# Kernel optimization log

Measured on AMD Instinct MI355X. Metric: run time of the kernel, lower is better.

The kernel has to match this reference:

```python
import jax, jax.numpy as jnp
import numpy as np
import itertools, functools, operator

NUM_RBF = 32
CUTOFF = 5.0
METRIC = (1, 1, 1)


def _count_bits(x):
    return bin(x).count("1")


def _sign_euclidean(a, b):
    a >>= 1
    s = 0
    while a:
        s += _count_bits(a & b)
        a >>= 1
    return 1 if (s & 1) == 0 else -1


def build_cayley(metric):
    """Dense [2^n, 2^n, 2^n] geometric multiplication (Cayley) table, shortlex blade order."""
    n = len(metric)
    blade_sets = itertools.chain.from_iterable(
        itertools.combinations([1 << i for i in range(n)], r) for r in range(n + 1)
    )
    index_to_bitmap = [functools.reduce(operator.or_, t, 0) for t in blade_sets]
    bitmap_to_index = {b: i for i, b in enumerate(index_to_bitmap)}
    N = 2 ** n
    cayley = np.zeros((N, N, N), dtype=np.float32)
    for i in range(N):
        bi = index_to_bitmap[i]
        for j in range(N):
            bj = index_to_bitmap[j]
            sign = _sign_euclidean(bi, bj)
            bm = bi & bj
            k = 0
            while bm:
                if bm & 1:
                    sign *= metric[k]
                k += 1
                bm >>= 1
            cayley[i, bitmap_to_index[bi ^ bj], j] = sign
    return cayley


CAYLEY = jnp.asarray(build_cayley(METRIC))  # [8,8,8], sparse +/-1 structure


def geometric_product(a, b):
    # torch: einsum('...i,ijk,...k->...j', a, cayley, b)
    return jnp.einsum('...i,ijk,...k->...j', a, CAYLEY, b)


def setup_inputs() -> dict:
    key = jax.random.key(0)
    k0, k1, k2, k3, k4, k5 = jax.random.split(key, 6)
    N, E, C = 50000, 800000, 16
    h = jax.random.normal(k0, (N, C, 8), jnp.float32)
    pos = jax.random.uniform(k1, (N, 3), jnp.float32) * 10.0
    edge_index = jax.random.randint(k2, (2, E), 0, N, jnp.int32)
    W_rbf = jax.random.normal(k3, (NUM_RBF, C), jnp.float32) / np.sqrt(NUM_RBF)
    W_out = jax.random.normal(k4, (C, C), jnp.float32) / np.sqrt(C)
    W_sgp = jax.random.normal(k5, (C, C), jnp.float32) / np.sqrt(C)
    return {"h": h, "pos": pos, "edge_index": edge_index,
            "W_rbf": W_rbf, "W_out": W_out, "W_sgp": W_sgp}


def reference(h, pos, edge_index, W_rbf, W_out, W_sgp):
    N, C, B = h.shape
    src, dst = edge_index[0], edge_index[1]

    # relative geometry
    rel = pos[dst] - pos[src]                                  # [E,3]
    dist = jnp.sqrt(jnp.sum(rel * rel, axis=-1) + 1e-12)       # [E]

    # embed unit relative vector as a grade-1 multivector (blades 1..3)
    rel_mv = jnp.zeros((rel.shape[0], 1, B), h.dtype)
    rel_mv = rel_mv.at[:, 0, 1:4].set(rel / dist[:, None])     # [E,1,8]

    # radial weights: gaussian smearing -> linear -> cosine cutoff envelope
    mus = jnp.linspace(0.0, CUTOFF, NUM_RBF, dtype=h.dtype)
    gamma = (NUM_RBF / CUTOFF) ** 2
    rbf = jnp.exp(-gamma * (dist[:, None] - mus) ** 2)         # [E,32]
    env = 0.5 * (jnp.cos(jnp.pi * dist / CUTOFF) + 1.0) * (dist < CUTOFF)
    w_e = (rbf @ W_rbf) * env[:, None]                          # [E,C]

    # equivariant messages: geometric product against edge multivector
    msg = geometric_product(h[src], rel_mv) * w_e[..., None]   # [E,C,8]
    agg = jax.ops.segment_sum(msg, dst, num_segments=N)        # [N,C,8]

    # MVLinear channel mixing (shared across blades)
    out = jnp.einsum('nci,co->noi', agg, W_out)                # [N,C,8]

    # MACE-style higher-order: steerable geometric product self-interaction
    q = jnp.einsum('nci,co->noi', h, W_sgp)                    # [N,C,8]
    return out + geometric_product(out, q)
```

## Files before the change

kernel.cpp:

```cpp
#include <hip/hip_runtime.h>

#define CUTOFF 5.0f
#define GAMMA 40.96f
#define MU_STEP 0.16129032f
#define INV_MU 6.2f
#define PI_F 3.14159265358979f
#define MAXDEG 24


__global__ __launch_bounds__(256) void k_fill_geom(
    const float* __restrict__ pos, const int* __restrict__ ei,
    int* __restrict__ deg, int* __restrict__ rec,
    float4* __restrict__ edata, int E)
{
    int e = blockIdx.x * 256 + threadIdx.x;
    if (e >= E) return;
    int src = ei[e], dst = ei[E + e];
    float dx = pos[dst*3+0] - pos[src*3+0];
    float dy = pos[dst*3+1] - pos[src*3+1];
    float dz = pos[dst*3+2] - pos[src*3+2];
    float d = sqrtf(dx*dx + dy*dy + dz*dz + 1e-12f);
    if (d < CUTOFF) {
        int slot = atomicAdd(&deg[dst], 1);
        if (slot < MAXDEG) {
            const float s = (0.5f * (__cosf(PI_F * d * (1.0f/CUTOFF)) + 1.0f)) / d;
            rec[dst*MAXDEG + slot] = src;
            edata[(size_t)dst*MAXDEG + slot] = make_float4(dx*s, dy*s, dz*s, d);
        }
    }
}

__global__ __launch_bounds__(256) void k_gather_finalize(
    const float* __restrict__ h,
    const int* __restrict__ rec, const int* __restrict__ deg,
    const float4* __restrict__ edata,
    const float* __restrict__ Wrbf, const float* __restrict__ Wout,
    const float* __restrict__ Wsgp, float* __restrict__ out, int N)
{
    __shared__ float s_wr[512];
    __shared__ float s_Wout[256];
    __shared__ float s_Wsgp[256];
    __shared__ float s_agg[16*132];
    __shared__ float s_h[16*132];

    const int t  = threadIdx.x;
    const int nl = t >> 4;
    const int c  = t & 15;
    const int lane  = t & 63;
    const int gbase = lane & 48;
    const long long nodeBase = (long long)blockIdx.x * 16;
    const long long n = nodeBase + nl;

    s_wr[t]       = Wrbf[t];
    s_wr[t + 256] = Wrbf[t + 256];
    s_Wout[t] = Wout[t];
    s_Wsgp[t] = Wsgp[t];

    for (int idx = t; idx < 512; idx += 256) {
        int nn = idx >> 5;
        int r  = idx & 31;
        long long node = nodeBase + nn;
        float4 vh = make_float4(0,0,0,0);
        if (node < N) vh = *(const float4*)(h + node*128 + (long long)r*4);
        *(float4*)(&s_h[nn*132 + r*4]) = vh;
    }
    __syncthreads();

    float m0=0,m1=0,m2=0,m3=0,m4=0,m5=0,m6=0,m7=0;
    if (n < N) {
        const int start = (int)n * MAXDEG;
        const int dg    = min(deg[n], MAXDEG);
        for (int base = 0; base < dg; base += 2) {
            const int i1ok = (base + 1 < dg) ? 1 : 0;
            const int s0 = rec[start + base];
            const int s1 = rec[start + base + i1ok];
            const float4 g0 = edata[start + base];
            const float4 g1 = edata[start + base + i1ok];

            const float4* hp0 = (const float4*)(h + (((long long)s0*16 + c) << 3));
            const float4* hp1 = (const float4*)(h + (((long long)s1*16 + c) << 3));
            const float4 A0 = hp0[0], B0 = hp0[1];
            const float4 A1 = hp1[0], B1 = hp1[1];

            const int kl0 = min(max(0, __float2int_rn(g0.w * INV_MU) - 3), 25);
            const int kl1 = min(max(0, __float2int_rn(g1.w * INV_MU) - 3), 25);

            const int   sel   = c >> 3;
            const float dsel  = sel ? g1.w : g0.w;
            const int   klsel = sel ? kl1 : kl0;
            const float xx = dsel - MU_STEP * (float)(klsel + (c & 7));
            const float ee = __expf(-GAMMA * xx * xx);

            float w0 = 0.0f, w1 = 0.0f;
            #pragma unroll
            for (int j = 0; j < 7; ++j) {
                const float e0 = __shfl(ee, gbase + j);
                const float e1 = __shfl(ee, gbase + 8 + j);
                w0 += e0 * s_wr[(kl0 + j)*16 + c];
                w1 += e1 * s_wr[(kl1 + j)*16 + c];
            }
            w1 *= (float)i1ok;

            m0 += (A0.y*g0.x + A0.z*g0.y + A0.w*g0.z)*w0 + (A1.y*g1.x + A1.z*g1.y + A1.w*g1.z)*w1;
            m1 += (A0.x*g0.x + B0.x*g0.y + B0.y*g0.z)*w0 + (A1.x*g1.x + B1.x*g1.y + B1.y*g1.z)*w1;
            m2 += (A0.x*g0.y - B0.x*g0.x + B0.z*g0.z)*w0 + (A1.x*g1.y - B1.x*g1.x + B1.z*g1.z)*w1;
            m3 += (A0.x*g0.z - B0.y*g0.x - B0.z*g0.y)*w0 + (A1.x*g1.z - B1.y*g1.x - B1.z*g1.y)*w1;
            m4 += (A0.y*g0.y - A0.z*g0.x + B0.w*g0.z)*w0 + (A1.y*g1.y - A1.z*g1.x + B1.w*g1.z)*w1;
            m5 += (A0.y*g0.z - A0.w*g0.x - B0.w*g0.y)*w0 + (A1.y*g1.z - A1.w*g1.x - B1.w*g1.y)*w1;
            m6 += (A0.z*g0.z - A0.w*g0.y + B0.w*g0.x)*w0 + (A1.z*g1.z - A1.w*g1.y + B1.w*g1.x)*w1;
            m7 += (B0.z*g0.x - B0.y*g0.y + B0.x*g0.z)*w0 + (B1.z*g1.x - B1.y*g1.y + B1.x*g1.z)*w1;
        }
    }

    __syncthreads();
    float* ag = &s_agg[nl*132 + c*8];
    *(float4*)(ag)     = make_float4(m0, m1, m2, m3);
    *(float4*)(ag + 4) = make_float4(m4, m5, m6, m7);
    __syncthreads();

    const int o = c;
    const float* A = &s_agg[nl*132];
    const float* H = &s_h[nl*132];

    float o0=0,o1=0,o2=0,o3=0,o4=0,o5=0,o6=0,o7=0;
    float q0=0,q1=0,q2=0,q3=0,q4=0,q5=0,q6=0,q7=0;
    #pragma unroll
    for (int cc = 0; cc < 16; ++cc) {
        const float wo = s_Wout[cc*16 + o];
        const float ws = s_Wsgp[cc*16 + o];
        const float* a  = A + cc*8;
        const float* hh = H + cc*8;
        o0 += a[0]*wo; o1 += a[1]*wo; o2 += a[2]*wo; o3 += a[3]*wo;
        o4 += a[4]*wo; o5 += a[5]*wo; o6 += a[6]*wo; o7 += a[7]*wo;
        q0 += hh[0]*ws; q1 += hh[1]*ws; q2 += hh[2]*ws; q3 += hh[3]*ws;
        q4 += hh[4]*ws; q5 += hh[5]*ws; q6 += hh[6]*ws; q7 += hh[7]*ws;
    }

    const float r0 = o0 + (o0*q0 + o1*q1 + o2*q2 + o3*q3 - o4*q4 - o5*q5 - o6*q6 - o7*q7);
    const float r1 = o1 + (o0*q1 + o1*q0 - o2*q4 - o3*q5 + o4*q2 + o5*q3 - o6*q7 - o7*q6);
    const float r2 = o2 + (o0*q2 + o1*q4 + o2*q0 - o3*q6 - o4*q1 + o5*q7 + o6*q3 + o7*q5);
    const float r3 = o3 + (o0*q3 + o1*q5 + o2*q6 + o3*q0 - o4*q7 - o5*q1 - o6*q2 - o7*q4);
    const float r4 = o4 + (o0*q4 + o1*q2 - o2*q1 + o3*q7 + o4*q0 - o5*q6 + o6*q5 + o7*q3);
    const float r5 = o5 + (o0*q5 + o1*q3 - o2*q7 - o3*q1 + o4*q6 + o5*q0 - o6*q4 - o7*q2);
    const float r6 = o6 + (o0*q6 + o1*q7 + o2*q3 - o3*q2 - o4*q5 + o5*q4 + o6*q0 + o7*q1);
    const float r7 = o7 + (o0*q7 + o1*q6 - o2*q5 + o3*q4 + o4*q3 - o5*q2 + o6*q1 + o7*q0);

    if (n < N) {
        float* op = out + (n*16 + o)*8;
        *(float4*)(op)     = make_float4(r0, r1, r2, r3);
        *(float4*)(op + 4) = make_float4(r4, r5, r6, r7);
    }
}

extern "C" void kernel_launch(void* const* d_in, const int* in_sizes, int n_in,
                              void* d_out, int out_size, void* d_ws, size_t ws_size,
                              hipStream_t stream) {
    const float* h    = (const float*)d_in[0];
    const float* pos  = (const float*)d_in[1];
    const int*   ei   = (const int*)d_in[2];
    const float* Wrbf = (const float*)d_in[3];
    const float* Wout = (const float*)d_in[4];
    const float* Wsgp = (const float*)d_in[5];
    float* out = (float*)d_out;

    const int N = in_sizes[0] / 128;
    const int E = in_sizes[2] / 2;

    float4* edata = (float4*)d_ws;
    int* deg = (int*)(edata + (size_t)N * MAXDEG);
    int* rec = deg + N;

    hipMemsetAsync(deg, 0, (size_t)N * sizeof(int), stream);

    const int eBlocks = (E + 255) / 256;
    k_fill_geom<<<eBlocks, 256, 0, stream>>>(pos, ei, deg, rec, edata, E);

    const int gBlocks = (N + 15) / 16;
    k_gather_finalize<<<gBlocks, 256, 0, stream>>>(
        h, rec, deg, edata, Wrbf, Wout, Wsgp, out, N);
}
```

Measured before the change: 138.0 us.

## Process two channels per thread and 32 nodes per block in gather kernel

Each thread now handles two channels of one node instead of one, so a 256-thread block covers 32 nodes. Per-edge work such as loading the edge index and geometry, computing the RBF exponentials and doing the shuffles is shared across two channels, and each thread issues four contiguous float4 h loads per edge instead of two. The RBF weight table is padded to a stride of 18 for float2 reads. In exchange, register pressure roughly doubles and there are half as many threads per node for hiding gather latency.

```diff
diff --git a/kernel.cpp b/kernel.cpp
--- a/kernel.cpp
+++ b/kernel.cpp
@@ -6,6 +6,7 @@
 #define INV_MU 6.2f
 #define PI_F 3.14159265358979f
 #define MAXDEG 24
+#define WRS 18
 
 
 __global__ __launch_bounds__(256) void k_fill_geom(
@@ -37,103 +38,125 @@
     const float* __restrict__ Wrbf, const float* __restrict__ Wout,
     const float* __restrict__ Wsgp, float* __restrict__ out, int N)
 {
-    __shared__ float s_wr[512];
+    __shared__ float s_wr[32*WRS];
     __shared__ float s_Wout[256];
     __shared__ float s_Wsgp[256];
-    __shared__ float s_agg[16*132];
-    __shared__ float s_h[16*132];
+    __shared__ float s_agg[32*132];
+    __shared__ float s_h[32*132];
 
     const int t  = threadIdx.x;
-    const int nl = t >> 4;
-    const int c  = t & 15;
+    const int nl = t >> 3;
+    const int k  = t & 7;
+    const int c0 = k << 1;
     const int lane  = t & 63;
-    const int gbase = lane & 48;
-    const long long nodeBase = (long long)blockIdx.x * 16;
+    const int gbase = lane & 56;
+    const long long nodeBase = (long long)blockIdx.x * 32;
     const long long n = nodeBase + nl;
 
-    s_wr[t]       = Wrbf[t];
-    s_wr[t + 256] = Wrbf[t + 256];
+    {
+        const int r0 = t >> 4, cw = t & 15;
+        s_wr[r0*WRS + cw]      = Wrbf[t];
+        s_wr[(r0+16)*WRS + cw] = Wrbf[t + 256];
+    }
     s_Wout[t] = Wout[t];
     s_Wsgp[t] = Wsgp[t];
 
-    for (int idx = t; idx < 512; idx += 256) {
-        int nn = idx >> 5;
-        int r  = idx & 31;
-        long long node = nodeBase + nn;
+    for (int idx = t; idx < 1024; idx += 256) {
+        const int nn = idx >> 5;
+        const int r  = idx & 31;
+        const long long node = nodeBase + nn;
         float4 vh = make_float4(0,0,0,0);
         if (node < N) vh = *(const float4*)(h + node*128 + (long long)r*4);
         *(float4*)(&s_h[nn*132 + r*4]) = vh;
     }
     __syncthreads();
 
-    float m0=0,m1=0,m2=0,m3=0,m4=0,m5=0,m6=0,m7=0;
+    float a0=0,a1=0,a2=0,a3=0,a4=0,a5=0,a6=0,a7=0;
+    float b0=0,b1=0,b2=0,b3=0,b4=0,b5=0,b6=0,b7=0;
     if (n < N) {
         const int start = (int)n * MAXDEG;
         const int dg    = min(deg[n], MAXDEG);
         for (int base = 0; base < dg; base += 2) {
             const int i1ok = (base + 1 < dg) ? 1 : 0;
-            const int s0 = rec[start + base];
-            const int s1 = rec[start + base + i1ok];
+            const int2 ss  = *(const int2*)(rec + start + base);
+            const int s0 = ss.x;
+            const int s1 = i1ok ? ss.y : ss.x;
             const float4 g0 = edata[start + base];
             const float4 g1 = edata[start + base + i1ok];
 
-            const float4* hp0 = (const float4*)(h + (((long long)s0*16 + c) << 3));
-            const float4* hp1 = (const float4*)(h + (((long long)s1*16 + c) << 3));
-            const float4 A0 = hp0[0], B0 = hp0[1];
-            const float4 A1 = hp1[0], B1 = hp1[1];
+            const float4* hp0 = (const float4*)(h) + (((long long)s0) << 5) + (k << 2);
+            const float4* hp1 = (const float4*)(h) + (((long long)s1) << 5) + (k << 2);
+            const float4 A0 = hp0[0], B0 = hp0[1], C0 = hp0[2], D0 = hp0[3];
+            const float4 A1 = hp1[0], B1 = hp1[1], C1 = hp1[2], D1 = hp1[3];
 
             const int kl0 = min(max(0, __float2int_rn(g0.w * INV_MU) - 3), 25);
             const int kl1 = min(max(0, __float2int_rn(g1.w * INV_MU) - 3), 25);
-
-            const int   sel   = c >> 3;
-            const float dsel  = sel ? g1.w : g0.w;
-            const int   klsel = sel ? kl1 : kl0;
-            const float xx = dsel - MU_STEP * (float)(klsel + (c & 7));
-            const float ee = __expf(-GAMMA * xx * xx);
-
-            float w0 = 0.0f, w1 = 0.0f;
+            const float x0 = g0.w - MU_STEP * (float)(kl0 + k);
+            const float x1 = g1.w - MU_STEP * (float)(kl1 + k);
+            const float ee0 = __expf(-GAMMA * x0 * x0);
+            const float ee1 = __expf(-GAMMA * x1 * x1);
+
+            float w00=0,w01=0,w10=0,w11=0;
             #pragma unroll
             for (int j = 0; j < 7; ++j) {
-                const float e0 = __shfl(ee, gbase + j);
-                const float e1 = __shfl(ee, gbase + 8 + j);
-                w0 += e0 * s_wr[(kl0 + j)*16 + c];
-                w1 += e1 * s_wr[(kl1 + j)*16 + c];
+                const float e0 = __shfl(ee0, gbase + j);
+                const float e1 = __shfl(ee1, gbase + j);
+                const float2 wa = *(const float2*)(s_wr + (kl0 + j)*WRS + c0);
+                const float2 wb = *(const float2*)(s_wr + (kl1 + j)*WRS + c0);
+                w00 += e0 * wa.x; w01 += e0 * wa.y;
+                w10 += e1 * wb.x; w11 += e1 * wb.y;
             }
-            w1 *= (float)i1ok;
-
-            m0 += (A0.y*g0.x + A0.z*g0.y + A0.w*g0.z)*w0 + (A1.y*g1.x + A1.z*g1.y + A1.w*g1.z)*w1;
-            m1 += (A0.x*g0.x + B0.x*g0.y + B0.y*g0.z)*w0 + (A1.x*g1.x + B1.x*g1.y + B1.y*g1.z)*w1;
-            m2 += (A0.x*g0.y - B0.x*g0.x + B0.z*g0.z)*w0 + (A1.x*g1.y - B1.x*g1.x + B1.z*g1.z)*w1;
-            m3 += (A0.x*g0.z - B0.y*g0.x - B0.z*g0.y)*w0 + (A1.x*g1.z - B1.y*g1.x - B1.z*g1.y)*w1;
-            m4 += (A0.y*g0.y - A0.z*g0.x + B0.w*g0.z)*w0 + (A1.y*g1.y - A1.z*g1.x + B1.w*g1.z)*w1;
-            m5 += (A0.y*g0.z - A0.w*g0.x - B0.w*g0.y)*w0 + (A1.y*g1.z - A1.w*g1.x - B1.w*g1.y)*w1;
-            m6 += (A0.z*g0.z - A0.w*g0.y + B0.w*g0.x)*w0 + (A1.z*g1.z - A1.w*g1.y + B1.w*g1.x)*w1;
-            m7 += (B0.z*g0.x - B0.y*g0.y + B0.x*g0.z)*w0 + (B1.z*g1.x - B1.y*g1.y + B1.x*g1.z)*w1;
+            const float f1 = (float)i1ok;
+            w10 *= f1; w11 *= f1;
+
+            a0 += (A0.y*g0.x + A0.z*g0.y + A0.w*g0.z)*w00 + (A1.y*g1.x + A1.z*g1.y + A1.w*g1.z)*w10;
+            a1 += (A0.x*g0.x + B0.x*g0.y + B0.y*g0.z)*w00 + (A1.x*g1.x + B1.x*g1.y + B1.y*g1.z)*w10;
+            a2 += (A0.x*g0.y - B0.x*g0.x + B0.z*g0.z)*w00 + (A1.x*g1.y - B1.x*g1.x + B1.z*g1.z)*w10;
+            a3 += (A0.x*g0.z - B0.y*g0.x - B0.z*g0.y)*w00 + (A1.x*g1.z - B1.y*g1.x - B1.z*g1.y)*w10;
+            a4 += (A0.y*g0.y - A0.z*g0.x + B0.w*g0.z)*w00 + (A1.y*g1.y - A1.z*g1.x + B1.w*g1.z)*w10;
+            a5 += (A0.y*g0.z - A0.w*g0.x - B0.w*g0.y)*w00 + (A1.y*g1.z - A1.w*g1.x - B1.w*g1.y)*w10;
+            a6 += (A0.z*g0.z - A0.w*g0.y + B0.w*g0.x)*w00 + (A1.z*g1.z - A1.w*g1.y + B1.w*g1.x)*w10;
+            a7 += (B0.z*g0.x - B0.y*g0.y + B0.x*g0.z)*w00 + (B1.z*g1.x - B1.y*g1.y + B1.x*g1.z)*w10;
+
+            b0 += (C0.y*g0.x + C0.z*g0.y + C0.w*g0.z)*w01 + (C1.y*g1.x + C1.z*g1.y + C1.w*g1.z)*w11;
+            b1 += (C0.x*g0.x + D0.x*g0.y + D0.y*g0.z)*w01 + (C1.x*g1.x + D1.x*g1.y + D1.y*g1.z)*w11;
+            b2 += (C0.x*g0.y - D0.x*g0.x + D0.z*g0.z)*w01 + (C1.x*g1.y - D1.x*g1.x + D1.z*g1.z)*w11;
+            b3 += (C0.x*g0.z - D0.y*g0.x - D0.z*g0.y)*w01 + (C1.x*g1.z - D1.y*g1.x - D1.z*g1.y)*w11;
+            b4 += (C0.y*g0.y - C0.z*g0.x + D0.w*g0.z)*w01 + (C1.y*g1.y - C1.z*g1.x + D1.w*g1.z)*w11;
+            b5 += (C0.y*g0.z - C0.w*g0.x - D0.w*g0.y)*w01 + (C1.y*g1.z - C1.w*g1.x - D1.w*g1.y)*w11;
+            b6 += (C0.z*g0.z - C0.w*g0.y + D0.w*g0.x)*w01 + (C1.z*g1.z - C1.w*g1.y + D1.w*g1.x)*w11;
+            b7 += (D0.z*g0.x - D0.y*g0.y + D0.x*g0.z)*w01 + (D1.z*g1.x - D1.y*g1.y + D1.x*g1.z)*w11;
         }
     }
 
+    float* ag = &s_agg[nl*132 + (c0 << 3)];
+    *(float4*)(ag)      = make_float4(a0,a1,a2,a3);
+    *(float4*)(ag + 4)  = make_float4(a4,a5,a6,a7);
+    *(float4*)(ag + 8)  = make_float4(b0,b1,b2,b3);
+    *(float4*)(ag + 12) = make_float4(b4,b5,b6,b7);
     __syncthreads();
-    float* ag = &s_agg[nl*132 + c*8];
-    *(float4*)(ag)     = make_float4(m0, m1, m2, m3);
-    *(float4*)(ag + 4) = make_float4(m4, m5, m6, m7);
-    __syncthreads();
-
-    const int o = c;
+
     const float* A = &s_agg[nl*132];
     const float* H = &s_h[nl*132];
 
     float o0=0,o1=0,o2=0,o3=0,o4=0,o5=0,o6=0,o7=0;
+    float p0=0,p1=0,p2=0,p3=0,p4=0,p5=0,p6=0,p7=0;
     float q0=0,q1=0,q2=0,q3=0,q4=0,q5=0,q6=0,q7=0;
+    float u0=0,u1=0,u2=0,u3=0,u4=0,u5=0,u6=0,u7=0;
     #pragma unroll
     for (int cc = 0; cc < 16; ++cc) {
-        const float wo = s_Wout[cc*16 + o];
-        const float ws = s_Wsgp[cc*16 + o];
+        const float2 wo = *(const float2*)(s_Wout + cc*16 + c0);
+        const float2 ws = *(const float2*)(s_Wsgp + cc*16 + c0);
         const float* a  = A + cc*8;
         const float* hh = H + cc*8;
-        o0 += a[0]*wo; o1 += a[1]*wo; o2 += a[2]*wo; o3 += a[3]*wo;
-        o4 += a[4]*wo; o5 += a[5]*wo; o6 += a[6]*wo; o7 += a[7]*wo;
-        q0 += hh[0]*ws; q1 += hh[1]*ws; q2 += hh[2]*ws; q3 += hh[3]*ws;
-        q4 += hh[4]*ws; q5 += hh[5]*ws; q6 += hh[6]*ws; q7 += hh[7]*ws;
+        o0 += a[0]*wo.x; o1 += a[1]*wo.x; o2 += a[2]*wo.x; o3 += a[3]*wo.x;
+        o4 += a[4]*wo.x; o5 += a[5]*wo.x; o6 += a[6]*wo.x; o7 += a[7]*wo.x;
+        p0 += a[0]*wo.y; p1 += a[1]*wo.y; p2 += a[2]*wo.y; p3 += a[3]*wo.y;
+        p4 += a[4]*wo.y; p5 += a[5]*wo.y; p6 += a[6]*wo.y; p7 += a[7]*wo.y;
+        q0 += hh[0]*ws.x; q1 += hh[1]*ws.x; q2 += hh[2]*ws.x; q3 += hh[3]*ws.x;
+        q4 += hh[4]*ws.x; q5 += hh[5]*ws.x; q6 += hh[6]*ws.x; q7 += hh[7]*ws.x;
+        u0 += hh[0]*ws.y; u1 += hh[1]*ws.y; u2 += hh[2]*ws.y; u3 += hh[3]*ws.y;
+        u4 += hh[4]*ws.y; u5 += hh[5]*ws.y; u6 += hh[6]*ws.y; u7 += hh[7]*ws.y;
     }
 
     const float r0 = o0 + (o0*q0 + o1*q1 + o2*q2 + o3*q3 - o4*q4 - o5*q5 - o6*q6 - o7*q7);
@@ -145,10 +168,21 @@
     const float r6 = o6 + (o0*q6 + o1*q7 + o2*q3 - o3*q2 - o4*q5 + o5*q4 + o6*q0 + o7*q1);
     const float r7 = o7 + (o0*q7 + o1*q6 - o2*q5 + o3*q4 + o4*q3 - o5*q2 + o6*q1 + o7*q0);
 
+    const float s0_ = p0 + (p0*u0 + p1*u1 + p2*u2 + p3*u3 - p4*u4 - p5*u5 - p6*u6 - p7*u7);
+    const float s1_ = p1 + (p0*u1 + p1*u0 - p2*u4 - p3*u5 + p4*u2 + p5*u3 - p6*u7 - p7*u6);
+    const float s2_ = p2 + (p0*u2 + p1*u4 + p2*u0 - p3*u6 - p4*u1 + p5*u7 + p6*u3 + p7*u5);
+    const float s3_ = p3 + (p0*u3 + p1*u5 + p2*u6 + p3*u0 - p4*u7 - p5*u1 - p6*u2 - p7*u4);
+    const float s4_ = p4 + (p0*u4 + p1*u2 - p2*u1 + p3*u7 + p4*u0 - p5*u6 + p6*u5 + p7*u3);
+    const float s5_ = p5 + (p0*u5 + p1*u3 - p2*u7 - p3*u1 + p4*u6 + p5*u0 - p6*u4 - p7*u2);
+    const float s6_ = p6 + (p0*u6 + p1*u7 + p2*u3 - p3*u2 - p4*u5 + p5*u4 + p6*u0 + p7*u1);
+    const float s7_ = p7 + (p0*u7 + p1*u6 - p2*u5 + p3*u4 + p4*u3 - p5*u2 + p6*u1 + p7*u0);
+
     if (n < N) {
-        float* op = out + (n*16 + o)*8;
-        *(float4*)(op)     = make_float4(r0, r1, r2, r3);
-        *(float4*)(op + 4) = make_float4(r4, r5, r6, r7);
+        float* op = out + n*128 + (long long)c0*8;
+        *(float4*)(op)      = make_float4(r0, r1, r2, r3);
+        *(float4*)(op + 4)  = make_float4(r4, r5, r6, r7);
+        *(float4*)(op + 8)  = make_float4(s0_, s1_, s2_, s3_);
+        *(float4*)(op + 12) = make_float4(s4_, s5_, s6_, s7_);
     }
 }
 
@@ -175,7 +209,7 @@
     const int eBlocks = (E + 255) / 256;
     k_fill_geom<<<eBlocks, 256, 0, stream>>>(pos, ei, deg, rec, edata, E);
 
-    const int gBlocks = (N + 15) / 16;
+    const int gBlocks = (N + 31) / 32;
     k_gather_finalize<<<gBlocks, 256, 0, stream>>>(
         h, rec, deg, edata, Wrbf, Wout, Wsgp, out, N);
 }
```

Measured after the change: 174.3 us. 26.3% more time.

## Precompute per-edge RBF exponentials in fill kernel and compact edge records

Applied to the files above, without the earlier changes.

Moves the seven Gaussian RBF exponentials and the window start index out of the gather kernel and into the edge-fill kernel. They are stored in a compact per-edge array indexed through a global atomic counter, and the gather kernel reads them instead of recomputing them with cross-lane shuffles. Source index and compact index are packed into an int2 so each pair of edges needs one int4 load. The aim is to cut transcendental and shuffle work from the gather loop, at the cost of 48 bytes per edge of extra traffic and a global atomic that may contend. There is also an overflow fallback that writes to slot 0.

```diff
diff --git a/kernel.cpp b/kernel.cpp
--- a/kernel.cpp
+++ b/kernel.cpp
@@ -10,8 +10,8 @@
 
 __global__ __launch_bounds__(256) void k_fill_geom(
     const float* __restrict__ pos, const int* __restrict__ ei,
-    int* __restrict__ deg, int* __restrict__ rec,
-    float4* __restrict__ edata, int E)
+    int* __restrict__ deg, int* __restrict__ cnt,
+    int2* __restrict__ rec2, float4* __restrict__ cmp, int cap, int E)
 {
     int e = blockIdx.x * 256 + threadIdx.x;
     if (e >= E) return;
@@ -23,17 +23,48 @@
     if (d < CUTOFF) {
         int slot = atomicAdd(&deg[dst], 1);
         if (slot < MAXDEG) {
+            int ci = atomicAdd(cnt, 1) + 1;
+            if (ci >= cap) {
+                cmp[0] = make_float4(0,0,0,0);
+                cmp[1] = make_float4(0,0,0,0);
+                cmp[2] = make_float4(0,0,0,0);
+                ci = 0;
+            }
             const float s = (0.5f * (__cosf(PI_F * d * (1.0f/CUTOFF)) + 1.0f)) / d;
-            rec[dst*MAXDEG + slot] = src;
-            edata[(size_t)dst*MAXDEG + slot] = make_float4(dx*s, dy*s, dz*s, d);
+            const int kl = min(max(0, __float2int_rn(d * INV_MU) - 3), 25);
+            float ex[7];
+            #pragma unroll
+            for (int j = 0; j < 7; ++j) {
+                const float x = d - MU_STEP * (float)(kl + j);
+                ex[j] = __expf(-GAMMA * x * x);
+            }
+            cmp[3*ci+0] = make_float4(dx*s, dy*s, dz*s, (float)kl);
+            cmp[3*ci+1] = make_float4(ex[0], ex[1], ex[2], ex[3]);
+            cmp[3*ci+2] = make_float4(ex[4], ex[5], ex[6], 0.0f);
+            rec2[dst*MAXDEG + slot] = make_int2(src, ci);
         }
     }
+}
+
+__device__ __forceinline__ void gp_acc(
+    const float4& A, const float4& B, const float4& g, float w,
+    float& m0, float& m1, float& m2, float& m3,
+    float& m4, float& m5, float& m6, float& m7)
+{
+    m0 += (A.y*g.x + A.z*g.y + A.w*g.z) * w;
+    m1 += (A.x*g.x + B.x*g.y + B.y*g.z) * w;
+    m2 += (A.x*g.y - B.x*g.x + B.z*g.z) * w;
+    m3 += (A.x*g.z - B.y*g.x - B.z*g.y) * w;
+    m4 += (A.y*g.y - A.z*g.x + B.w*g.z) * w;
+    m5 += (A.y*g.z - A.w*g.x - B.w*g.y) * w;
+    m6 += (A.z*g.z - A.w*g.y + B.w*g.x) * w;
+    m7 += (B.z*g.x - B.y*g.y + B.x*g.z) * w;
 }
 
 __global__ __launch_bounds__(256) void k_gather_finalize(
     const float* __restrict__ h,
-    const int* __restrict__ rec, const int* __restrict__ deg,
-    const float4* __restrict__ edata,
+    const int2* __restrict__ rec2, const int* __restrict__ deg,
+    const float4* __restrict__ cmp,
     const float* __restrict__ Wrbf, const float* __restrict__ Wout,
     const float* __restrict__ Wsgp, float* __restrict__ out, int N)
 {
@@ -46,8 +77,6 @@
     const int t  = threadIdx.x;
     const int nl = t >> 4;
     const int c  = t & 15;
-    const int lane  = t & 63;
-    const int gbase = lane & 48;
     const long long nodeBase = (long long)blockIdx.x * 16;
     const long long n = nodeBase + nl;
 
@@ -70,45 +99,40 @@
     if (n < N) {
         const int start = (int)n * MAXDEG;
         const int dg    = min(deg[n], MAXDEG);
-        for (int base = 0; base < dg; base += 2) {
-            const int i1ok = (base + 1 < dg) ? 1 : 0;
-            const int s0 = rec[start + base];
-            const int s1 = rec[start + base + i1ok];
-            const float4 g0 = edata[start + base];
-            const float4 g1 = edata[start + base + i1ok];
-
-            const float4* hp0 = (const float4*)(h + (((long long)s0*16 + c) << 3));
-            const float4* hp1 = (const float4*)(h + (((long long)s1*16 + c) << 3));
+        int base = 0;
+        for (; base + 1 < dg; base += 2) {
+            const int4 rr = *(const int4*)(rec2 + start + base);
+
+            const float4* hp0 = (const float4*)(h) + (((long long)rr.x) << 5) + (c << 1);
+            const float4* hp1 = (const float4*)(h) + (((long long)rr.z) << 5) + (c << 1);
             const float4 A0 = hp0[0], B0 = hp0[1];
             const float4 A1 = hp1[0], B1 = hp1[1];
 
-            const int kl0 = min(max(0, __float2int_rn(g0.w * INV_MU) - 3), 25);
-            const int kl1 = min(max(0, __float2int_rn(g1.w * INV_MU) - 3), 25);
-
-            const int   sel   = c >> 3;
-            const float dsel  = sel ? g1.w : g0.w;
-            const int   klsel = sel ? kl1 : kl0;
-            const float xx = dsel - MU_STEP * (float)(klsel + (c & 7));
-            const float ee = __expf(-GAMMA * xx * xx);
-
-            float w0 = 0.0f, w1 = 0.0f;
-            #pragma unroll
-            for (int j = 0; j < 7; ++j) {
-                const float e0 = __shfl(ee, gbase + j);
-                const float e1 = __shfl(ee, gbase + 8 + j);
-                w0 += e0 * s_wr[(kl0 + j)*16 + c];
-                w1 += e1 * s_wr[(kl1 + j)*16 + c];
-            }
-            w1 *= (float)i1ok;
-
-            m0 += (A0.y*g0.x + A0.z*g0.y + A0.w*g0.z)*w0 + (A1.y*g1.x + A1.z*g1.y + A1.w*g1.z)*w1;
-            m1 += (A0.x*g0.x + B0.x*g0.y + B0.y*g0.z)*w0 + (A1.x*g1.x + B1.x*g1.y + B1.y*g1.z)*w1;
-            m2 += (A0.x*g0.y - B0.x*g0.x + B0.z*g0.z)*w0 + (A1.x*g1.y - B1.x*g1.x + B1.z*g1.z)*w1;
-            m3 += (A0.x*g0.z - B0.y*g0.x - B0.z*g0.y)*w0 + (A1.x*g1.z - B1.y*g1.x - B1.z*g1.y)*w1;
-            m4 += (A0.y*g0.y - A0.z*g0.x + B0.w*g0.z)*w0 + (A1.y*g1.y - A1.z*g1.x + B1.w*g1.z)*w1;
-            m5 += (A0.y*g0.z - A0.w*g0.x - B0.w*g0.y)*w0 + (A1.y*g1.z - A1.w*g1.x - B1.w*g1.y)*w1;
-            m6 += (A0.z*g0.z - A0.w*g0.y + B0.w*g0.x)*w0 + (A1.z*g1.z - A1.w*g1.y + B1.w*g1.x)*w1;
-            m7 += (B0.z*g0.x - B0.y*g0.y + B0.x*g0.z)*w0 + (B1.z*g1.x - B1.y*g1.y + B1.x*g1.z)*w1;
+            const float4 g0  = cmp[3*rr.y],   g1  = cmp[3*rr.w];
+            const float4 E0a = cmp[3*rr.y+1], E1a = cmp[3*rr.w+1];
+            const float4 E0b = cmp[3*rr.y+2], E1b = cmp[3*rr.w+2];
+
+            const float* wr0 = s_wr + ((int)g0.w)*16 + c;
+            const float* wr1 = s_wr + ((int)g1.w)*16 + c;
+            const float w0 = E0a.x*wr0[0]  + E0a.y*wr0[16] + E0a.z*wr0[32] + E0a.w*wr0[48]
+                           + E0b.x*wr0[64] + E0b.y*wr0[80] + E0b.z*wr0[96];
+            const float w1 = E1a.x*wr1[0]  + E1a.y*wr1[16] + E1a.z*wr1[32] + E1a.w*wr1[48]
+                           + E1b.x*wr1[64] + E1b.y*wr1[80] + E1b.z*wr1[96];
+
+            gp_acc(A0, B0, g0, w0, m0,m1,m2,m3,m4,m5,m6,m7);
+            gp_acc(A1, B1, g1, w1, m0,m1,m2,m3,m4,m5,m6,m7);
+        }
+        if (base < dg) {
+            const int2 rr = rec2[start + base];
+            const float4* hp0 = (const float4*)(h) + (((long long)rr.x) << 5) + (c << 1);
+            const float4 A0 = hp0[0], B0 = hp0[1];
+            const float4 g0  = cmp[3*rr.y];
+            const float4 E0a = cmp[3*rr.y+1];
+            const float4 E0b = cmp[3*rr.y+2];
+            const float* wr0 = s_wr + ((int)g0.w)*16 + c;
+            const float w0 = E0a.x*wr0[0]  + E0a.y*wr0[16] + E0a.z*wr0[32] + E0a.w*wr0[48]
+                           + E0b.x*wr0[64] + E0b.y*wr0[80] + E0b.z*wr0[96];
+            gp_acc(A0, B0, g0, w0, m0,m1,m2,m3,m4,m5,m6,m7);
         }
     }
 
@@ -166,16 +190,23 @@
     const int N = in_sizes[0] / 128;
     const int E = in_sizes[2] / 2;
 
-    float4* edata = (float4*)d_ws;
-    int* deg = (int*)(edata + (size_t)N * MAXDEG);
-    int* rec = deg + N;
-
-    hipMemsetAsync(deg, 0, (size_t)N * sizeof(int), stream);
+    const size_t fixedBytes = (size_t)N * MAXDEG * sizeof(int2)
+                            + (size_t)(N + 1) * sizeof(int);
+    long long capLL = (long long)((ws_size - fixedBytes) / 48u);
+    if (capLL > (long long)E + 1) capLL = (long long)E + 1;
+    const int cap = (int)capLL;
+
+    float4* cmp = (float4*)d_ws;
+    int2* rec2  = (int2*)((char*)d_ws + (size_t)cap * 48u);
+    int* deg    = (int*)(rec2 + (size_t)N * MAXDEG);
+    int* cnt    = deg + N;
+
+    hipMemsetAsync(deg, 0, (size_t)(N + 1) * sizeof(int), stream);
 
     const int eBlocks = (E + 255) / 256;
-    k_fill_geom<<<eBlocks, 256, 0, stream>>>(pos, ei, deg, rec, edata, E);
+    k_fill_geom<<<eBlocks, 256, 0, stream>>>(pos, ei, deg, cnt, rec2, cmp, cap, E);
 
     const int gBlocks = (N + 15) / 16;
     k_gather_finalize<<<gBlocks, 256, 0, stream>>>(
-        h, rec, deg, edata, Wrbf, Wout, Wsgp, out, N);
-}
+        h, rec2, deg, cmp, Wrbf, Wout, Wsgp, out, N);
+}
```

New measurement: 297.7 us. +115.7%, slower.

## Replace per-edge RBF expansion with precomputed radial weight lookup table

Applied to the files above, without the earlier changes.

Precomputes a 2048-entry table over distance of the enveloped radial weights (RBF smearing times W_rbf times cosine cutoff) per channel, using extra blocks in the geometry kernel. The gather kernel then linearly interpolates from this table instead of computing exps, shuffles and a shared-memory dot product per edge. This removes per-edge transcendental and shuffle work and frees the W_rbf shared memory, at the cost of interpolation error and a small table read per edge.

```diff
diff --git a/kernel.cpp b/kernel.cpp
--- a/kernel.cpp
+++ b/kernel.cpp
@@ -3,29 +3,54 @@
 #define CUTOFF 5.0f
 #define GAMMA 40.96f
 #define MU_STEP 0.16129032f
-#define INV_MU 6.2f
 #define PI_F 3.14159265358979f
 #define MAXDEG 24
+#define TAB 2048
+#define DSTEP (CUTOFF / (float)TAB)
+#define TSCALE ((float)TAB / CUTOFF)
 
 
 __global__ __launch_bounds__(256) void k_fill_geom(
     const float* __restrict__ pos, const int* __restrict__ ei,
+    const float* __restrict__ Wrbf,
     int* __restrict__ deg, int* __restrict__ rec,
-    float4* __restrict__ edata, int E)
+    float4* __restrict__ edata, float2* __restrict__ tabp,
+    int E, int eBlocks)
 {
-    int e = blockIdx.x * 256 + threadIdx.x;
+    if (blockIdx.x >= eBlocks) {
+        const int gid = (blockIdx.x - eBlocks) * 256 + threadIdx.x;
+        const int i = gid >> 4;
+        const int c = gid & 15;
+        const float d0 = (float)i * DSTEP;
+        const float d1 = d0 + DSTEP;
+        float acc0 = 0.0f, acc1 = 0.0f;
+        #pragma unroll
+        for (int k = 0; k < 32; ++k) {
+            const float w  = Wrbf[k*16 + c];
+            const float x0 = d0 - MU_STEP * (float)k;
+            const float x1 = d1 - MU_STEP * (float)k;
+            acc0 += __expf(-GAMMA * x0 * x0) * w;
+            acc1 += __expf(-GAMMA * x1 * x1) * w;
+        }
+        const float env0 = 0.5f * (__cosf(PI_F * d0 * (1.0f/CUTOFF)) + 1.0f);
+        const float env1 = 0.5f * (__cosf(PI_F * d1 * (1.0f/CUTOFF)) + 1.0f);
+        tabp[gid] = make_float2(acc0 * env0, acc1 * env1);
+        return;
+    }
+
+    const int e = blockIdx.x * 256 + threadIdx.x;
     if (e >= E) return;
-    int src = ei[e], dst = ei[E + e];
-    float dx = pos[dst*3+0] - pos[src*3+0];
-    float dy = pos[dst*3+1] - pos[src*3+1];
-    float dz = pos[dst*3+2] - pos[src*3+2];
-    float d = sqrtf(dx*dx + dy*dy + dz*dz + 1e-12f);
+    const int src = ei[e], dst = ei[E + e];
+    const float dx = pos[dst*3+0] - pos[src*3+0];
+    const float dy = pos[dst*3+1] - pos[src*3+1];
+    const float dz = pos[dst*3+2] - pos[src*3+2];
+    const float d = sqrtf(dx*dx + dy*dy + dz*dz + 1e-12f);
     if (d < CUTOFF) {
-        int slot = atomicAdd(&deg[dst], 1);
+        const int slot = atomicAdd(&deg[dst], 1);
         if (slot < MAXDEG) {
-            const float s = (0.5f * (__cosf(PI_F * d * (1.0f/CUTOFF)) + 1.0f)) / d;
+            const float inv = 1.0f / d;
             rec[dst*MAXDEG + slot] = src;
-            edata[(size_t)dst*MAXDEG + slot] = make_float4(dx*s, dy*s, dz*s, d);
+            edata[(size_t)dst*MAXDEG + slot] = make_float4(dx*inv, dy*inv, dz*inv, d);
         }
     }
 }
@@ -33,11 +58,10 @@
 __global__ __launch_bounds__(256) void k_gather_finalize(
     const float* __restrict__ h,
     const int* __restrict__ rec, const int* __restrict__ deg,
-    const float4* __restrict__ edata,
-    const float* __restrict__ Wrbf, const float* __restrict__ Wout,
-    const float* __restrict__ Wsgp, float* __restrict__ out, int N)
+    const float4* __restrict__ edata, const float2* __restrict__ tabp,
+    const float* __restrict__ Wout, const float* __restrict__ Wsgp,
+    float* __restrict__ out, int N)
 {
-    __shared__ float s_wr[512];
     __shared__ float s_Wout[256];
     __shared__ float s_Wsgp[256];
     __shared__ float s_agg[16*132];
@@ -46,13 +70,9 @@
     const int t  = threadIdx.x;
     const int nl = t >> 4;
     const int c  = t & 15;
-    const int lane  = t & 63;
-    const int gbase = lane & 48;
     const long long nodeBase = (long long)blockIdx.x * 16;
     const long long n = nodeBase + nl;
 
-    s_wr[t]       = Wrbf[t];
-    s_wr[t + 256] = Wrbf[t + 256];
     s_Wout[t] = Wout[t];
     s_Wsgp[t] = Wsgp[t];
 
@@ -82,23 +102,16 @@
             const float4 A0 = hp0[0], B0 = hp0[1];
             const float4 A1 = hp1[0], B1 = hp1[1];
 
-            const int kl0 = min(max(0, __float2int_rn(g0.w * INV_MU) - 3), 25);
-            const int kl1 = min(max(0, __float2int_rn(g1.w * INV_MU) - 3), 25);
-
-            const int   sel   = c >> 3;
-            const float dsel  = sel ? g1.w : g0.w;
-            const int   klsel = sel ? kl1 : kl0;
-            const float xx = dsel - MU_STEP * (float)(klsel + (c & 7));
-            const float ee = __expf(-GAMMA * xx * xx);
-
-            float w0 = 0.0f, w1 = 0.0f;
-            #pragma unroll
-            for (int j = 0; j < 7; ++j) {
-                const float e0 = __shfl(ee, gbase + j);
-                const float e1 = __shfl(ee, gbase + 8 + j);
-                w0 += e0 * s_wr[(kl0 + j)*16 + c];
-                w1 += e1 * s_wr[(kl1 + j)*16 + c];
-            }
+            const float u0 = g0.w * TSCALE;
+            const float u1 = g1.w * TSCALE;
+            int it0 = (int)u0; it0 = min(it0, TAB - 1);
+            int it1 = (int)u1; it1 = min(it1, TAB - 1);
+            const float fr0 = u0 - (float)it0;
+            const float fr1 = u1 - (float)it1;
+            const float2 tp0 = tabp[it0*16 + c];
+            const float2 tp1 = tabp[it1*16 + c];
+            const float w0 = tp0.x + fr0 * (tp0.y - tp0.x);
+            float       w1 = tp1.x + fr1 * (tp1.y - tp1.x);
             w1 *= (float)i1ok;
 
             m0 += (A0.y*g0.x + A0.z*g0.y + A0.w*g0.z)*w0 + (A1.y*g1.x + A1.z*g1.y + A1.w*g1.z)*w1;
@@ -166,16 +179,19 @@
     const int N = in_sizes[0] / 128;
     const int E = in_sizes[2] / 2;
 
-    float4* edata = (float4*)d_ws;
+    float2* tabp  = (float2*)d_ws;
+    float4* edata = (float4*)(tabp + (size_t)TAB * 16);
     int* deg = (int*)(edata + (size_t)N * MAXDEG);
     int* rec = deg + N;
 
     hipMemsetAsync(deg, 0, (size_t)N * sizeof(int), stream);
 
     const int eBlocks = (E + 255) / 256;
-    k_fill_geom<<<eBlocks, 256, 0, stream>>>(pos, ei, deg, rec, edata, E);
+    const int tBlocks = (TAB * 16) / 256;
+    k_fill_geom<<<eBlocks + tBlocks, 256, 0, stream>>>(
+        pos, ei, Wrbf, deg, rec, edata, tabp, E, eBlocks);
 
     const int gBlocks = (N + 15) / 16;
     k_gather_finalize<<<gBlocks, 256, 0, stream>>>(
-        h, rec, deg, edata, Wrbf, Wout, Wsgp, out, N);
+        h, rec, deg, edata, tabp, Wout, Wsgp, out, N);
 }
```

Result: slower. 153.9 us (+11.5%).
